# Kernel optimization log

Measured on AMD Instinct MI355X. Metric: run time of the kernel, lower is better.

## Reference

```python
import jax, jax.numpy as jnp
import numpy as np
import math

B, S, D, H, KVH, HD = 1, 2048, 4096, 32, 8, 128
N_REP = H // KVH


def _rope_tables(seq_len, half_dim):
    # standard RoPE angle table: theta_{p,i} = p / 10000^(2i/HD)
    inv_freq = 1.0 / (10000.0 ** (np.arange(0, half_dim, dtype=np.float32) / half_dim))
    angles = np.arange(seq_len, dtype=np.float32)[:, None] * inv_freq[None, :]
    return jnp.asarray(np.cos(angles)), jnp.asarray(np.sin(angles))


def setup_inputs() -> dict:
    key = jax.random.key(0)
    ks = jax.random.split(key, 5)
    scale = 0.02
    x = jax.random.normal(ks[0], (B, S, D), dtype=jnp.float32)
    wq = jax.random.normal(ks[1], (D, H * HD), dtype=jnp.float32) * scale
    wk = jax.random.normal(ks[2], (D, KVH * HD), dtype=jnp.float32) * scale
    wv = jax.random.normal(ks[3], (D, KVH * HD), dtype=jnp.float32) * scale
    wo = jax.random.normal(ks[4], (H * HD, D), dtype=jnp.float32) * scale
    cache_k = jnp.zeros((B, S, KVH, HD), dtype=jnp.float32)
    cache_v = jnp.zeros((B, S, KVH, HD), dtype=jnp.float32)
    freqs_cos, freqs_sin = _rope_tables(S, HD // 2)  # [S, HD//2]
    # causal mask, broadcast onto scores [B, H, S, S]
    mask = jnp.triu(jnp.full((S, S), -1e9, dtype=jnp.float32), k=1)
    input_indexes = jnp.arange(S, dtype=jnp.int32)
    return {"x": x, "wq": wq, "wk": wk, "wv": wv, "wo": wo,
            "cache_k": cache_k, "cache_v": cache_v,
            "freqs_cos": freqs_cos, "freqs_sin": freqs_sin,
            "mask": mask, "input_indexes": input_indexes}


def _apply_rope(t, cos, sin):
    # t: [B, S, h, HD]; consecutive pairs (even=real, odd=imag), matching
    # torch.view_as_complex on reshape(..., HD//2, 2)
    tr, ti = t[..., 0::2], t[..., 1::2]            # [B, S, h, HD//2]
    c = cos[None, :, None, :]
    s = sin[None, :, None, :]
    out_r = tr * c - ti * s
    out_i = tr * s + ti * c
    return jnp.stack([out_r, out_i], axis=-1).reshape(t.shape)


def reference(x, wq, wk, wv, wo, cache_k, cache_v, freqs_cos, freqs_sin, mask, input_indexes):
    bsz, seqlen, _ = x.shape
    xq = (x @ wq).reshape(bsz, seqlen, H, HD)
    xk = (x @ wk).reshape(bsz, seqlen, KVH, HD)
    xv = (x @ wv).reshape(bsz, seqlen, KVH, HD)

    xq = _apply_rope(xq, freqs_cos, freqs_sin)
    xk = _apply_rope(xk, freqs_cos, freqs_sin)

    # KV-cache update (index_copy along dim 1)
    keys = cache_k.at[:, input_indexes].set(xk)    # [B, S, KVH, HD]
    values = cache_v.at[:, input_indexes].set(xv)  # [B, S, KVH, HD]

    # GQA: implicit broadcast of KV heads instead of physical repeat_kv
    q = xq.reshape(bsz, seqlen, KVH, N_REP, HD)
    scores = jnp.einsum('bqkrd,bskd->bkrqs', q, keys) / math.sqrt(HD)
    scores = scores.reshape(bsz, H, seqlen, S) + mask[None, None]
    probs = jax.nn.softmax(scores.astype(jnp.float32), axis=-1).astype(x.dtype)
    probs = probs.reshape(bsz, KVH, N_REP, seqlen, S)
    out = jnp.einsum('bkrqs,bskd->bqkrd', probs, values)
    out = out.reshape(bsz, seqlen, H * HD)
    return out @ wo
```

## Files before the change

### kernel.cpp

```cpp
#include <hip/hip_runtime.h>
#include <hip/hip_bf16.h>


constexpr int S_LEN  = 2048;
constexpr int DMODEL = 4096;
constexpr int NH     = 32;
constexpr int NKV    = 8;
constexpr int HDIM   = 128;
constexpr int QKVN   = 6144;
constexpr int KCOL   = 4096;
constexpr int VCOL   = 5120;

typedef __attribute__((ext_vector_type(8))) short short8;
typedef __attribute__((ext_vector_type(4))) float f32x4;

__device__ __forceinline__ ushort f2bf(float f) {
  uint u = __builtin_bit_cast(uint, f);
  u = (u + 0x7fffu + ((u >> 16) & 1u)) >> 16;
  return (ushort)u;
}
__device__ __forceinline__ uint pk2(float a, float b) {
  return (uint)f2bf(a) | ((uint)f2bf(b) << 16);
}
__device__ __forceinline__ float2 bf2f2(uint u) {
  uint lo = u << 16, hi = u & 0xffff0000u;
  return make_float2(__builtin_bit_cast(float, lo), __builtin_bit_cast(float, hi));
}
__device__ __forceinline__ short8 ldfrag(const ushort* p) {
  union { short8 v; uint2 u[2]; } f;
  f.u[0] = *(const uint2*)p;
  f.u[1] = *(const uint2*)(p + 4);
  return f.v;
}
__device__ __forceinline__ short8 u4s8(uint4 u) {
  return __builtin_bit_cast(short8, u);
}

template<bool A_IS_F32, bool OUT_BF16, bool FUSED>
__launch_bounds__(256)
__global__ void gemm_mfma(const void* __restrict__ Av, int lda,
                          const float* __restrict__ Bq,
                          const float* __restrict__ Bk,
                          const float* __restrict__ Bv, int ldb0,
                          void* __restrict__ Cv, int ldc, int K) {
  __shared__ ushort AsU[128 * 68];
  __shared__ ushort BsU[128 * 68];
  const int tid = threadIdx.x;
  const int lane = tid & 63;
  const int w = tid >> 6;
  const int wr = w >> 1, wc = w & 1;
  const int ln = lane & 15, lg = lane >> 4;
  const int row0 = blockIdx.y * 128;
  const int col0 = blockIdx.x * 128;

  const float* B;
  int nb, ldb;
  if constexpr (FUSED) {
    if (col0 < KCOL)      { B = Bq; nb = col0;        ldb = DMODEL; }
    else if (col0 < VCOL) { B = Bk; nb = col0 - KCOL; ldb = 1024;   }
    else                  { B = Bv; nb = col0 - VCOL; ldb = 1024;   }
  } else {
    B = Bq; nb = col0; ldb = ldb0;
  }

  const int rA  = tid >> 4, cA4 = tid & 15;
  const int rA2 = tid >> 3, cA8 = tid & 7;
  const int ngB = tid & 31, kgB = tid >> 5;

  float aRf[8][4];
  uint4 aRu[4];
  float bRa[2][4][4];

  auto LOAD = [&](int k0) {
    if constexpr (A_IS_F32) {
      const float* Af = (const float*)Av;
#pragma unroll
      for (int i = 0; i < 8; ++i) {
        float4 t4 = *(const float4*)(Af + (size_t)(row0 + rA + 16 * i) * lda + k0 + 4 * cA4);
        aRf[i][0] = t4.x; aRf[i][1] = t4.y; aRf[i][2] = t4.z; aRf[i][3] = t4.w;
      }
    } else {
      const ushort* Ah = (const ushort*)Av;
#pragma unroll
      for (int i = 0; i < 4; ++i)
        aRu[i] = *(const uint4*)(Ah + (size_t)(row0 + rA2 + 32 * i) * lda + k0 + 8 * cA8);
    }
#pragma unroll
    for (int g = 0; g < 2; ++g) {
      int kg = kgB + 8 * g;
#pragma unroll
      for (int j = 0; j < 4; ++j) {
        float4 t4 = *(const float4*)(B + (size_t)(k0 + 4 * kg + j) * ldb + nb + 4 * ngB);
        bRa[g][j][0] = t4.x; bRa[g][j][1] = t4.y; bRa[g][j][2] = t4.z; bRa[g][j][3] = t4.w;
      }
    }
  };

  auto WRITE = [&]() {
    if constexpr (A_IS_F32) {
#pragma unroll
      for (int i = 0; i < 8; ++i) {
        int r = rA + 16 * i;
        *(uint2*)&AsU[r * 68 + 4 * cA4] =
            make_uint2(pk2(aRf[i][0], aRf[i][1]), pk2(aRf[i][2], aRf[i][3]));
      }
    } else {
#pragma unroll
      for (int i = 0; i < 4; ++i) {
        int r = rA2 + 32 * i;
        *(uint2*)&AsU[r * 68 + 8 * cA8]     = make_uint2(aRu[i].x, aRu[i].y);
        *(uint2*)&AsU[r * 68 + 8 * cA8 + 4] = make_uint2(aRu[i].z, aRu[i].w);
      }
    }
#pragma unroll
    for (int g = 0; g < 2; ++g) {
      int kg = kgB + 8 * g;
#pragma unroll
      for (int c = 0; c < 4; ++c) {
        int r = 4 * ngB + c;
        *(uint2*)&BsU[r * 68 + 4 * kg] =
            make_uint2(pk2(bRa[g][0][c], bRa[g][1][c]), pk2(bRa[g][2][c], bRa[g][3][c]));
      }
    }
  };

  f32x4 acc[4][4];
#pragma unroll
  for (int mt = 0; mt < 4; ++mt)
#pragma unroll
    for (int nt = 0; nt < 4; ++nt) acc[mt][nt] = (f32x4)0.f;

  const int aBase = (wr * 64 + ln) * 68 + lg * 8;
  const int bBase = (wc * 64 + ln) * 68 + lg * 8;

  LOAD(0);
  const int nT = K >> 6;
  for (int t = 0; t < nT; ++t) {
    __syncthreads();
    WRITE();
    __syncthreads();
    if (t + 1 < nT) LOAD((t + 1) * 64);
#pragma unroll
    for (int kk = 0; kk < 64; kk += 32) {
      short8 af[4], bfr[4];
#pragma unroll
      for (int mt = 0; mt < 4; ++mt) af[mt] = ldfrag(&AsU[aBase + mt * 16 * 68 + kk]);
#pragma unroll
      for (int nt = 0; nt < 4; ++nt) bfr[nt] = ldfrag(&BsU[bBase + nt * 16 * 68 + kk]);
#pragma unroll
      for (int mt = 0; mt < 4; ++mt)
#pragma unroll
        for (int nt = 0; nt < 4; ++nt)
          acc[mt][nt] = __builtin_amdgcn_mfma_f32_16x16x32_bf16(af[mt], bfr[nt], acc[mt][nt], 0, 0, 0);
    }
  }

#pragma unroll
  for (int mt = 0; mt < 4; ++mt)
#pragma unroll
    for (int nt = 0; nt < 4; ++nt)
#pragma unroll
      for (int r = 0; r < 4; ++r) {
        size_t grow = row0 + wr * 64 + mt * 16 + lg * 4 + r;
        size_t gcol = col0 + wc * 64 + nt * 16 + ln;
        float v = acc[mt][nt][r];
        if constexpr (OUT_BF16) ((ushort*)Cv)[grow * ldc + gcol] = f2bf(v);
        else                    ((float*)Cv)[grow * ldc + gcol] = v;
      }
}

constexpr int ROPE_NQ = S_LEN * NH * (HDIM / 2);
constexpr int ROPE_NK = S_LEN * NKV * (HDIM / 2);

__launch_bounds__(256)
__global__ void rope_qk(ushort* __restrict__ xqkv,
                        const float* __restrict__ fcos, const float* __restrict__ fsin) {
  int t = blockIdx.x * 256 + threadIdx.x;
  ushort* p;
  int s, i;
  float scale;
  if (t < ROPE_NQ) {
    i = t & 63;
    int hh = (t >> 6) & 31;
    s = t >> 11;
    p = xqkv + (size_t)s * QKVN + hh * HDIM + 2 * i;
    scale = 0.08838834764831845f;
  } else {
    int u = t - ROPE_NQ;
    i = u & 63;
    int hh = (u >> 6) & 7;
    s = u >> 9;
    p = xqkv + (size_t)s * QKVN + KCOL + hh * HDIM + 2 * i;
    scale = 1.0f;
  }
  float c = fcos[s * 64 + i];
  float sn = fsin[s * 64 + i];
  float2 v = bf2f2(*(const uint*)p);
  *(uint*)p = pk2((v.x * c - v.y * sn) * scale, (v.x * sn + v.y * c) * scale);
}

__launch_bounds__(256)
__global__ void vtrans(const ushort* __restrict__ xqkv, ushort* __restrict__ vt) {
  __shared__ ushort T[128 * 68];
  const int s0 = blockIdx.x * 64;
  const int kvh = blockIdx.y;
  const int tid = threadIdx.x;
  const int s = tid & 63;
  const int d8 = tid >> 6;
  const ushort* src = xqkv + (size_t)(s0 + s) * QKVN + VCOL + kvh * HDIM;
#pragma unroll
  for (int p = 0; p < 4; ++p) {
    int dblk = (d8 + 4 * p) * 8;
    uint4 u = *(const uint4*)(src + dblk);
    uint ws[4] = {u.x, u.y, u.z, u.w};
#pragma unroll
    for (int j = 0; j < 4; ++j) {
      T[(dblk + 2 * j) * 68 + s]     = (ushort)(ws[j] & 0xffffu);
      T[(dblk + 2 * j + 1) * 68 + s] = (ushort)(ws[j] >> 16);
    }
  }
  __syncthreads();
  const int d = tid >> 1;
  const int sh = tid & 1;
  const ushort* trow = T + d * 68 + sh * 32;
  uint2 a0 = *(const uint2*)(trow + 0),  a1 = *(const uint2*)(trow + 4);
  uint2 a2 = *(const uint2*)(trow + 8),  a3 = *(const uint2*)(trow + 12);
  uint2 a4 = *(const uint2*)(trow + 16), a5 = *(const uint2*)(trow + 20);
  uint2 a6 = *(const uint2*)(trow + 24), a7 = *(const uint2*)(trow + 28);
  ushort* dst = vt + ((size_t)kvh * 128 + d) * 2048 + s0 + sh * 32;
  *(uint4*)(dst + 0)  = make_uint4(a0.x, a0.y, a1.x, a1.y);
  *(uint4*)(dst + 8)  = make_uint4(a2.x, a2.y, a3.x, a3.y);
  *(uint4*)(dst + 16) = make_uint4(a4.x, a4.y, a5.x, a5.y);
  *(uint4*)(dst + 24) = make_uint4(a6.x, a6.y, a7.x, a7.y);
}

__launch_bounds__(256)
__global__ void attn_mfma(const ushort* __restrict__ xqkv,
                          const ushort* __restrict__ vt,
                          ushort* __restrict__ abuf) {
  __shared__ ushort Pw[4][16 * 68];
  const int b = blockIdx.x;
  const int h = blockIdx.y;
  const int kvh = h >> 2;
  const int tid = threadIdx.x;
  const int lane = tid & 63;
  const int w = tid >> 6;
  const int ln = lane & 15, lg = lane >> 4;
  ushort* pw = Pw[w];

#pragma unroll 1
  for (int phase = 0; phase < 2; ++phase) {
    const int qt = phase ? (31 - b) : b;
    const int qr = qt * 64 + w * 16;
    short8 qf[4];
    {
      const ushort* qp = xqkv + (size_t)(qr + ln) * QKVN + h * HDIM + lg * 8;
#pragma unroll
      for (int kf = 0; kf < 4; ++kf) qf[kf] = u4s8(*(const uint4*)(qp + kf * 32));
    }
    float m[4], l[4];
    f32x4 oacc[8];
#pragma unroll
    for (int r = 0; r < 4; ++r) { m[r] = -1e30f; l[r] = 0.f; }
#pragma unroll
    for (int nf = 0; nf < 8; ++nf) oacc[nf] = (f32x4)0.f;

    for (int kt = 0; kt <= qt; ++kt) {
      f32x4 sacc[4];
#pragma unroll
      for (int nf = 0; nf < 4; ++nf) sacc[nf] = (f32x4)0.f;
      const ushort* kp = xqkv + (size_t)(kt * 64 + ln) * QKVN + KCOL + kvh * HDIM + lg * 8;
#pragma unroll
      for (int nf = 0; nf < 4; ++nf) {
        const ushort* kr = kp + (size_t)(nf * 16) * QKVN;
        uint4 b0 = *(const uint4*)(kr);
        uint4 b1 = *(const uint4*)(kr + 32);
        uint4 b2 = *(const uint4*)(kr + 64);
        uint4 b3 = *(const uint4*)(kr + 96);
        sacc[nf] = __builtin_amdgcn_mfma_f32_16x16x32_bf16(qf[0], u4s8(b0), sacc[nf], 0, 0, 0);
        sacc[nf] = __builtin_amdgcn_mfma_f32_16x16x32_bf16(qf[1], u4s8(b1), sacc[nf], 0, 0, 0);
        sacc[nf] = __builtin_amdgcn_mfma_f32_16x16x32_bf16(qf[2], u4s8(b2), sacc[nf], 0, 0, 0);
        sacc[nf] = __builtin_amdgcn_mfma_f32_16x16x32_bf16(qf[3], u4s8(b3), sacc[nf], 0, 0, 0);
      }
      if (kt == qt) {
        const int qcd = w * 16 + 4 * lg;
#pragma unroll
        for (int nf = 0; nf < 4; ++nf)
#pragma unroll
          for (int r = 0; r < 4; ++r)
            if (nf * 16 + ln > qcd + r) sacc[nf][r] = -1e30f;
      }
      float mx[4];
#pragma unroll
      for (int r = 0; r < 4; ++r) {
        float v = fmaxf(fmaxf(sacc[0][r], sacc[1][r]), fmaxf(sacc[2][r], sacc[3][r]));
#pragma unroll
        for (int off = 1; off < 16; off <<= 1) v = fmaxf(v, __shfl_xor(v, off));
        mx[r] = v;
      }
      float need = 0.f;
#pragma unroll
      for (int r = 0; r < 4; ++r) need = fmaxf(need, mx[r] - m[r]);
      if (!__all(need <= 8.f)) {
#pragma unroll
        for (int r = 0; r < 4; ++r) {
          float nm = fmaxf(m[r], mx[r]);
          float f = __expf(m[r] - nm);
          m[r] = nm; l[r] *= f;
#pragma unroll
          for (int nf = 0; nf < 8; ++nf) oacc[nf][r] *= f;
        }
      }
#pragma unroll
      for (int nf = 0; nf < 4; ++nf)
#pragma unroll
        for (int r = 0; r < 4; ++r) {
          float p = __expf(sacc[nf][r] - m[r]);
          l[r] += p;
          pw[(4 * lg + r) * 68 + nf * 16 + ln] = f2bf(p);
        }
      short8 pa0 = ldfrag(pw + ln * 68 + lg * 8);
      short8 pa1 = ldfrag(pw + ln * 68 + 32 + lg * 8);
      const ushort* vp = vt + ((size_t)kvh * 128 + ln) * 2048 + kt * 64 + lg * 8;
#pragma unroll
      for (int nf = 0; nf < 8; ++nf) {
        const ushort* vr = vp + (size_t)(nf * 16) * 2048;
        uint4 v0 = *(const uint4*)(vr);
        uint4 v1 = *(const uint4*)(vr + 32);
        oacc[nf] = __builtin_amdgcn_mfma_f32_16x16x32_bf16(pa0, u4s8(v0), oacc[nf], 0, 0, 0);
        oacc[nf] = __builtin_amdgcn_mfma_f32_16x16x32_bf16(pa1, u4s8(v1), oacc[nf], 0, 0, 0);
      }
    }
#pragma unroll
    for (int r = 0; r < 4; ++r) {
#pragma unroll
      for (int off = 1; off < 16; off <<= 1) l[r] += __shfl_xor(l[r], off);
      l[r] = 1.f / l[r];
    }
    ushort* op = abuf + (size_t)(qr + 4 * lg) * DMODEL + h * HDIM + ln;
#pragma unroll
    for (int nf = 0; nf < 8; ++nf)
#pragma unroll
      for (int r = 0; r < 4; ++r)
        op[(size_t)r * DMODEL + nf * 16] = f2bf(oacc[nf][r] * l[r]);
  }
}

extern "C" void kernel_launch(void* const* d_in, const int* in_sizes, int n_in,
                              void* d_out, int out_size, void* d_ws, size_t ws_size,
                              hipStream_t stream) {
  (void)in_sizes; (void)n_in; (void)out_size; (void)ws_size;
  const float* x    = (const float*)d_in[0];
  const float* wq   = (const float*)d_in[1];
  const float* wk   = (const float*)d_in[2];
  const float* wv   = (const float*)d_in[3];
  const float* wo   = (const float*)d_in[4];
  const float* fcos = (const float*)d_in[7];
  const float* fsin = (const float*)d_in[8];
  float* out = (float*)d_out;

  ushort* xqkv = (ushort*)d_ws;
  ushort* abuf = xqkv + (size_t)S_LEN * QKVN;
  ushort* vt = (ushort*)d_out;

  gemm_mfma<true, true, true><<<dim3(QKVN / 128, S_LEN / 128), 256, 0, stream>>>(
      x, DMODEL, wq, wk, wv, 0, xqkv, QKVN, DMODEL);
  rope_qk<<<(ROPE_NQ + ROPE_NK) / 256, 256, 0, stream>>>(xqkv, fcos, fsin);
  vtrans<<<dim3(S_LEN / 64, NKV), 256, 0, stream>>>(xqkv, vt);
  attn_mfma<<<dim3(16, NH), 256, 0, stream>>>(xqkv, vt, abuf);
  gemm_mfma<false, false, false><<<dim3(DMODEL / 128, S_LEN / 128), 256, 0, stream>>>(
      abuf, DMODEL, wo, nullptr, nullptr, DMODEL, out, DMODEL, DMODEL);
}
```

Before: 780.3 us.

## Pre-convert inputs to bf16 and transposed weights, use LDS-direct bf16 GEMM

Adds kernels that convert x to bf16 and transpose-convert each weight matrix to a bf16 N-major layout in workspace. A new GEMM then streams both operands into shared memory with global_load_lds 16-byte loads and uses 16x16x32 bf16 MFMA. The goal is to drop the fp32 load and in-loop conversion from the main GEMM loops. In exchange it adds extra conversion passes over about 100M weight elements on every call, and the new path only runs when the workspace is large enough, otherwise the old path is used.

```diff
diff --git a/kernel.cpp b/kernel.cpp
--- a/kernel.cpp
+++ b/kernel.cpp
@@ -32,8 +32,115 @@
   f.u[1] = *(const uint2*)(p + 4);
   return f.v;
 }
+__device__ __forceinline__ short8 ldfrag16(const ushort* p) {
+  return __builtin_bit_cast(short8, *(const uint4*)p);
+}
 __device__ __forceinline__ short8 u4s8(uint4 u) {
   return __builtin_bit_cast(short8, u);
+}
+typedef __attribute__((address_space(1))) const void GAS;
+typedef __attribute__((address_space(3))) void LAS;
+__device__ __forceinline__ void gl_lds16(const ushort* g, ushort* l) {
+  __builtin_amdgcn_global_load_lds((GAS*)g, (LAS*)l, 16, 0, 0);
+}
+
+__launch_bounds__(256)
+__global__ void cvt_bf16(const float* __restrict__ src, ushort* __restrict__ dst) {
+  size_t i = ((size_t)blockIdx.x * 256 + threadIdx.x) * 8;
+  float4 a = *(const float4*)(src + i);
+  float4 b = *(const float4*)(src + i + 4);
+  *(uint4*)(dst + i) = make_uint4(pk2(a.x, a.y), pk2(a.z, a.w),
+                                  pk2(b.x, b.y), pk2(b.z, b.w));
+}
+
+__launch_bounds__(256)
+__global__ void wtrans(const float* __restrict__ src, int N,
+                       ushort* __restrict__ dst) {
+  __shared__ ushort T[64][68];
+  const int k0 = blockIdx.x * 64, n0 = blockIdx.y * 64;
+  const int tid = threadIdx.x;
+  const int kr = tid >> 4, c4 = (tid & 15) * 4;
+#pragma unroll
+  for (int i = 0; i < 4; ++i) {
+    float4 v = *(const float4*)(src + (size_t)(k0 + kr + 16 * i) * N + n0 + c4);
+    T[c4 + 0][kr + 16 * i] = f2bf(v.x);
+    T[c4 + 1][kr + 16 * i] = f2bf(v.y);
+    T[c4 + 2][kr + 16 * i] = f2bf(v.z);
+    T[c4 + 3][kr + 16 * i] = f2bf(v.w);
+  }
+  __syncthreads();
+  const int nr = tid >> 2, kc = (tid & 3) * 16;
+  ushort* d = dst + (size_t)(n0 + nr) * 4096 + k0 + kc;
+  *(uint2*)(d + 0)  = *(const uint2*)&T[nr][kc + 0];
+  *(uint2*)(d + 4)  = *(const uint2*)&T[nr][kc + 4];
+  *(uint2*)(d + 8)  = *(const uint2*)&T[nr][kc + 8];
+  *(uint2*)(d + 12) = *(const uint2*)&T[nr][kc + 12];
+}
+
+template<bool OUT_BF16>
+__launch_bounds__(256)
+__global__ void gemm_bt(const ushort* __restrict__ A,
+                        const ushort* __restrict__ BT,
+                        void* __restrict__ Cv, int ldc, int K) {
+  __shared__ ushort As[128 * 64];
+  __shared__ ushort Bs[128 * 64];
+  const int tid = threadIdx.x;
+  const int lane = tid & 63;
+  const int w = tid >> 6;
+  const int wr = w >> 1, wc = w & 1;
+  const int ln = lane & 15, lg = lane >> 4;
+  const int row0 = blockIdx.y * 128;
+  const int col0 = blockIdx.x * 128;
+  const int srow = lane >> 3;
+  const int sslot = lane & 7;
+
+  f32x4 acc[4][4];
+#pragma unroll
+  for (int mt = 0; mt < 4; ++mt)
+#pragma unroll
+    for (int nt = 0; nt < 4; ++nt) acc[mt][nt] = (f32x4)0.f;
+
+  const ushort* Ab = A + (size_t)row0 * K;
+  const ushort* Bb = BT + (size_t)col0 * K;
+
+  for (int k0 = 0; k0 < K; k0 += 64) {
+    __syncthreads();
+#pragma unroll
+    for (int c = 0; c < 4; ++c) {
+      const int ch = w * 4 + c;
+      gl_lds16(Ab + (size_t)(ch * 8 + srow) * K + k0 + sslot * 8, &As[ch * 512]);
+      gl_lds16(Bb + (size_t)(ch * 8 + srow) * K + k0 + sslot * 8, &Bs[ch * 512]);
+    }
+    __syncthreads();
+#pragma unroll
+    for (int kk = 0; kk < 64; kk += 32) {
+      short8 af[4], bfr[4];
+#pragma unroll
+      for (int mt = 0; mt < 4; ++mt)
+        af[mt] = ldfrag16(&As[(wr * 64 + mt * 16 + ln) * 64 + kk + lg * 8]);
+#pragma unroll
+      for (int nt = 0; nt < 4; ++nt)
+        bfr[nt] = ldfrag16(&Bs[(wc * 64 + nt * 16 + ln) * 64 + kk + lg * 8]);
+#pragma unroll
+      for (int mt = 0; mt < 4; ++mt)
+#pragma unroll
+        for (int nt = 0; nt < 4; ++nt)
+          acc[mt][nt] = __builtin_amdgcn_mfma_f32_16x16x32_bf16(af[mt], bfr[nt], acc[mt][nt], 0, 0, 0);
+    }
+  }
+
+#pragma unroll
+  for (int mt = 0; mt < 4; ++mt)
+#pragma unroll
+    for (int nt = 0; nt < 4; ++nt)
+#pragma unroll
+      for (int r = 0; r < 4; ++r) {
+        size_t grow = row0 + wr * 64 + mt * 16 + lg * 4 + r;
+        size_t gcol = col0 + wc * 64 + nt * 16 + ln;
+        float v = acc[mt][nt][r];
+        if constexpr (OUT_BF16) ((ushort*)Cv)[grow * ldc + gcol] = f2bf(v);
+        else                    ((float*)Cv)[grow * ldc + gcol] = v;
+      }
 }
 
 template<bool A_IS_F32, bool OUT_BF16, bool FUSED>
@@ -349,7 +456,7 @@
 extern "C" void kernel_launch(void* const* d_in, const int* in_sizes, int n_in,
                               void* d_out, int out_size, void* d_ws, size_t ws_size,
                               hipStream_t stream) {
-  (void)in_sizes; (void)n_in; (void)out_size; (void)ws_size;
+  (void)in_sizes; (void)n_in; (void)out_size;
   const float* x    = (const float*)d_in[0];
   const float* wq   = (const float*)d_in[1];
   const float* wk   = (const float*)d_in[2];
@@ -363,11 +470,32 @@
   ushort* abuf = xqkv + (size_t)S_LEN * QKVN;
   ushort* vt = (ushort*)d_out;
 
-  gemm_mfma<true, true, true><<<dim3(QKVN / 128, S_LEN / 128), 256, 0, stream>>>(
-      x, DMODEL, wq, wk, wv, 0, xqkv, QKVN, DMODEL);
-  rope_qk<<<(ROPE_NQ + ROPE_NK) / 256, 256, 0, stream>>>(xqkv, fcos, fsin);
-  vtrans<<<dim3(S_LEN / 64, NKV), 256, 0, stream>>>(xqkv, vt);
-  attn_mfma<<<dim3(16, NH), 256, 0, stream>>>(xqkv, vt, abuf);
-  gemm_mfma<false, false, false><<<dim3(DMODEL / 128, S_LEN / 128), 256, 0, stream>>>(
-      abuf, DMODEL, wo, nullptr, nullptr, DMODEL, out, DMODEL, DMODEL);
-}
+  const size_t FAST_WS = (size_t)S_LEN * QKVN * 2 + (size_t)S_LEN * DMODEL * 2 +
+                         (size_t)QKVN * DMODEL * 2;
+
+  if (ws_size >= FAST_WS) {
+    ushort* xbf = abuf;
+    ushort* WT  = abuf + (size_t)S_LEN * DMODEL;
+
+    cvt_bf16<<<(S_LEN * DMODEL) / (256 * 8), 256, 0, stream>>>(x, xbf);
+    wtrans<<<dim3(64, 64), 256, 0, stream>>>(wq, DMODEL, WT);
+    wtrans<<<dim3(64, 16), 256, 0, stream>>>(wk, 1024, WT + (size_t)KCOL * DMODEL);
+    wtrans<<<dim3(64, 16), 256, 0, stream>>>(wv, 1024, WT + (size_t)VCOL * DMODEL);
+    gemm_bt<true><<<dim3(QKVN / 128, S_LEN / 128), 256, 0, stream>>>(
+        xbf, WT, xqkv, QKVN, DMODEL);
+    wtrans<<<dim3(64, 64), 256, 0, stream>>>(wo, DMODEL, WT);
+    rope_qk<<<(ROPE_NQ + ROPE_NK) / 256, 256, 0, stream>>>(xqkv, fcos, fsin);
+    vtrans<<<dim3(S_LEN / 64, NKV), 256, 0, stream>>>(xqkv, vt);
+    attn_mfma<<<dim3(16, NH), 256, 0, stream>>>(xqkv, vt, abuf);
+    gemm_bt<false><<<dim3(DMODEL / 128, S_LEN / 128), 256, 0, stream>>>(
+        abuf, WT, out, DMODEL, DMODEL);
+  } else {
+    gemm_mfma<true, true, true><<<dim3(QKVN / 128, S_LEN / 128), 256, 0, stream>>>(
+        x, DMODEL, wq, wk, wv, 0, xqkv, QKVN, DMODEL);
+    rope_qk<<<(ROPE_NQ + ROPE_NK) / 256, 256, 0, stream>>>(xqkv, fcos, fsin);
+    vtrans<<<dim3(S_LEN / 64, NKV), 256, 0, stream>>>(xqkv, vt);
+    attn_mfma<<<dim3(16, NH), 256, 0, stream>>>(xqkv, vt, abuf);
+    gemm_mfma<false, false, false><<<dim3(DMODEL / 128, S_LEN / 128), 256, 0, stream>>>(
+        abuf, DMODEL, wo, nullptr, nullptr, DMODEL, out, DMODEL, DMODEL);
+  }
+}
```

Measured after the change: 772.2 us. Within noise of the previous version (-1.0%).
